# Kernel tuning notes

Hardware: AMD Instinct MI355X
Metric: run time of the kernel (lower is better)

Reference implementation:

```python
import jax, jax.numpy as jnp
import numpy as np

B, DIN, HID, DOUT, E, TOPK = 8192, 1024, 2048, 1024, 8, 2
GHID = HID // 2  # gating hidden


def setup_inputs() -> dict:
    key = jax.random.key(0)
    ks = jax.random.split(key, 16)
    s = lambda fan_in: 1.0 / np.sqrt(fan_in)
    return {
        "x": jax.random.normal(ks[0], (B, DIN), dtype=jnp.float32),
        # stacked expert params, leading axis = expert
        "w1": jax.random.uniform(ks[1], (E, DIN, HID), jnp.float32, -s(DIN), s(DIN)),
        "b1": jax.random.uniform(ks[2], (E, HID), jnp.float32, -s(DIN), s(DIN)),
        "w2": jax.random.uniform(ks[3], (E, HID, HID), jnp.float32, -s(HID), s(HID)),
        "b2": jax.random.uniform(ks[4], (E, HID), jnp.float32, -s(HID), s(HID)),
        "w3": jax.random.uniform(ks[5], (E, HID, DOUT), jnp.float32, -s(HID), s(HID)),
        "b3": jax.random.uniform(ks[6], (E, DOUT), jnp.float32, -s(HID), s(HID)),
        "wp": jax.random.uniform(ks[7], (E, DIN, HID), jnp.float32, -s(DIN), s(DIN)),
        "bp": jax.random.uniform(ks[8], (E, HID), jnp.float32, -s(DIN), s(DIN)),
        # gating network: Linear(DIN, GHID) -> ReLU -> Linear(GHID, E)
        "gw1": jax.random.uniform(ks[9], (DIN, GHID), jnp.float32, -s(DIN), s(DIN)),
        "gb1": jax.random.uniform(ks[10], (GHID,), jnp.float32, -s(DIN), s(DIN)),
        "gw2": jax.random.uniform(ks[11], (GHID, E), jnp.float32, -s(GHID), s(GHID)),
        "gb2": jax.random.uniform(ks[12], (E,), jnp.float32, -s(GHID), s(GHID)),
    }


def reference(x, w1, b1, w2, b2, w3, b3, wp, bp, gw1, gb1, gw2, gb2):
    # gating: [B, E]
    gate_logits = jnp.maximum(x @ gw1 + gb1, 0.0) @ gw2 + gb2
    topk_w, topk_i = jax.lax.top_k(gate_logits, TOPK)  # [B, K]
    topk_w = jax.nn.softmax(topk_w, axis=1)
    # dense per-expert residual MLP (dropout is identity in eval mode)
    h = jnp.maximum(jnp.einsum('bi,eih->beh', x, w1) + b1, 0.0)  # [B,E,HID]
    out = jnp.einsum('beh,ehg->beg', h, w2) + b2                  # [B,E,HID]
    identity = jnp.einsum('bi,eih->beh', x, wp) + bp              # projection
    out = jnp.maximum(out + identity, 0.0)
    expert_out = jnp.einsum('beh,eho->beo', out, w3) + b3         # [B,E,DOUT]
    # scatter top-k weights into dense [B, E] gate
    gate = jnp.zeros_like(gate_logits).at[jnp.arange(x.shape[0])[:, None], topk_i].set(topk_w)
    return jnp.einsum('beo,be->bo', expert_out, gate)             # [B, DOUT]
```

## Files before the change

### kernel.cpp

```cpp
#include <hip/hip_runtime.h>
#include <hip/hip_bf16.h>
#include <cstdint>
#include <cstddef>

#define TOK  8192
#define DIN  1024
#define HID  2048
#define DOUTN 1024
#define NEXP 8
#define GHID 1024

typedef __attribute__((ext_vector_type(8))) short bf16x8;
typedef __attribute__((ext_vector_type(4))) float floatx4;

__device__ __forceinline__ unsigned short f2b(float f) {
  unsigned int u = __float_as_uint(f);
  u += 0x7fffu + ((u >> 16) & 1u);
  return (unsigned short)(u >> 16);
}

__device__ __forceinline__ void async_cp16(const unsigned short* g, char* lds) {
  __builtin_amdgcn_global_load_lds(
      (const __attribute__((address_space(1))) unsigned int*)g,
      (__attribute__((address_space(3))) unsigned int*)lds, 16, 0, 0);
}


__global__ void cvt_x_kernel(const float* __restrict__ src,
                             unsigned short* __restrict__ dst, int n4) {
  int i = blockIdx.x * blockDim.x + threadIdx.x;
  if (i >= n4) return;
  float4 v = ((const float4*)src)[i];
  ushort4 o;
  o.x = f2b(v.x); o.y = f2b(v.y); o.z = f2b(v.z); o.w = f2b(v.w);
  ((ushort4*)dst)[i] = o;
}

__global__ void cvt_transpose_kernel(const float* __restrict__ src,
                                     unsigned short* __restrict__ dst,
                                     int K, int N) {
  __shared__ float tile[32][33];
  long e = blockIdx.z;
  src += e * (long)K * N;
  dst += e * (long)K * N;
  int n0 = blockIdx.x * 32, k0 = blockIdx.y * 32;
  int x = threadIdx.x, y = threadIdx.y;
#pragma unroll
  for (int i = 0; i < 4; i++)
    tile[y + 8 * i][x] = src[(long)(k0 + y + 8 * i) * N + n0 + x];
  __syncthreads();
#pragma unroll
  for (int i = 0; i < 4; i++)
    dst[(long)(n0 + y + 8 * i) * K + k0 + x] = f2b(tile[x][y + 8 * i]);
}


__global__ __launch_bounds__(256) void gating_sgemm(
    const float* __restrict__ X, const float* __restrict__ W,
    const float* __restrict__ bias, float* __restrict__ H) {
  __shared__ float As[8][128];
  __shared__ float Bs[8][128];
  int tid = threadIdx.x;
  int bm = blockIdx.y, bn = blockIdx.x;
  int tx = tid & 15, ty = tid >> 4;

  float acc[8][8] = {};
  int arow = tid >> 1;
  int acol = (tid & 1) * 4;
  int brow = tid >> 5;
  int bcol = (tid & 31) * 4;
  const float* Xp = X + (size_t)(bm * 128 + arow) * DIN + acol;
  const float* Wp = W + (size_t)brow * GHID + bn * 128 + bcol;

  for (int k0 = 0; k0 < DIN; k0 += 8) {
    float4 av = *(const float4*)(Xp + k0);
    float4 bv = *(const float4*)(Wp + (size_t)k0 * GHID);
    __syncthreads();
    As[acol + 0][arow] = av.x;
    As[acol + 1][arow] = av.y;
    As[acol + 2][arow] = av.z;
    As[acol + 3][arow] = av.w;
    *(float4*)&Bs[brow][bcol] = bv;
    __syncthreads();
#pragma unroll
    for (int k = 0; k < 8; ++k) {
      float ar[8], br[8];
      *(float4*)&ar[0] = *(const float4*)&As[k][ty * 4];
      *(float4*)&ar[4] = *(const float4*)&As[k][64 + ty * 4];
      *(float4*)&br[0] = *(const float4*)&Bs[k][tx * 4];
      *(float4*)&br[4] = *(const float4*)&Bs[k][64 + tx * 4];
#pragma unroll
      for (int i = 0; i < 8; ++i)
#pragma unroll
        for (int j = 0; j < 8; ++j) acc[i][j] += ar[i] * br[j];
    }
  }

#pragma unroll
  for (int hn = 0; hn < 2; ++hn) {
    int c0 = bn * 128 + hn * 64 + tx * 4;
    float4 bb = *(const float4*)(bias + c0);
#pragma unroll
    for (int hm = 0; hm < 2; ++hm)
#pragma unroll
      for (int i = 0; i < 4; ++i) {
        int m = bm * 128 + hm * 64 + ty * 4 + i;
        float4 v;
        v.x = fmaxf(acc[hm * 4 + i][hn * 4 + 0] + bb.x, 0.f);
        v.y = fmaxf(acc[hm * 4 + i][hn * 4 + 1] + bb.y, 0.f);
        v.z = fmaxf(acc[hm * 4 + i][hn * 4 + 2] + bb.z, 0.f);
        v.w = fmaxf(acc[hm * 4 + i][hn * 4 + 3] + bb.w, 0.f);
        *(float4*)(H + (size_t)m * GHID + c0) = v;
      }
  }
}


__global__ void gating2_topk(const float* __restrict__ H,
                             const float* __restrict__ gw2,
                             const float* __restrict__ gb2,
                             int* __restrict__ gidx, float* __restrict__ gwt) {
  int wv = threadIdx.x >> 6, lane = threadIdx.x & 63;
  int t = blockIdx.x * 4 + wv;
  const float* hrow = H + (size_t)t * GHID;
  float acc[8] = {};
  for (int k = lane; k < GHID; k += 64) {
    float v = hrow[k];
    float4 g0 = *(const float4*)(gw2 + (size_t)k * 8);
    float4 g1 = *(const float4*)(gw2 + (size_t)k * 8 + 4);
    acc[0] += v * g0.x; acc[1] += v * g0.y; acc[2] += v * g0.z; acc[3] += v * g0.w;
    acc[4] += v * g1.x; acc[5] += v * g1.y; acc[6] += v * g1.z; acc[7] += v * g1.w;
  }
#pragma unroll
  for (int off = 32; off > 0; off >>= 1)
#pragma unroll
    for (int e = 0; e < 8; e++) acc[e] += __shfl_xor(acc[e], off);

  if (lane == 0) {
    float l[8];
#pragma unroll
    for (int e = 0; e < 8; e++) l[e] = acc[e] + gb2[e];
    int b0 = 0; float v0 = l[0];
#pragma unroll
    for (int e = 1; e < 8; e++) if (l[e] > v0) { v0 = l[e]; b0 = e; }
    int b1 = -1; float v1 = -3.4e38f;
#pragma unroll
    for (int e = 0; e < 8; e++)
      if (e != b0 && l[e] > v1) { v1 = l[e]; b1 = e; }
    float ex = expf(v1 - v0);
    float inv = 1.f / (1.f + ex);
    gidx[2 * t] = b0; gidx[2 * t + 1] = b1;
    gwt[2 * t] = inv; gwt[2 * t + 1] = ex * inv;
  }
}


__global__ void route_count(const int* __restrict__ gidx, int* cnt) {
  int t = blockIdx.x * blockDim.x + threadIdx.x;
  int lane = threadIdx.x & 63;
  int e0 = gidx[2 * t], e1 = gidx[2 * t + 1];
#pragma unroll 1
  for (int e = 0; e < NEXP; e++) {
    unsigned long long m0 = __ballot(e0 == e);
    if (m0 && lane == __ffsll(m0) - 1) atomicAdd(&cnt[e], (int)__popcll(m0));
    unsigned long long m1 = __ballot(e1 == e);
    if (m1 && lane == __ffsll(m1) - 1) atomicAdd(&cnt[e], (int)__popcll(m1));
  }
}

__global__ void route_scan(const int* __restrict__ cnt, int* base_, int* cur) {
  if (threadIdx.x == 0) {
    int s = 0;
    for (int e = 0; e < NEXP; e++) { base_[e] = s; cur[e] = s; s += cnt[e]; }
  }
}

__global__ void route_scatter(const int* __restrict__ gidx,
                              const float* __restrict__ gwt, int* cur,
                              int* __restrict__ rt, float* __restrict__ rw) {
  int t = blockIdx.x * blockDim.x + threadIdx.x;
  int lane = threadIdx.x & 63;
  int e0 = gidx[2 * t], e1 = gidx[2 * t + 1];
  float w0 = gwt[2 * t], w1 = gwt[2 * t + 1];
#pragma unroll 1
  for (int e = 0; e < NEXP; e++) {
#pragma unroll 1
    for (int s = 0; s < 2; s++) {
      int mye = s ? e1 : e0;
      unsigned long long m = __ballot(mye == e);
      if (m) {
        int leader = __ffsll(m) - 1;
        int bb = 0;
        if (lane == leader) bb = atomicAdd(&cur[e], (int)__popcll(m));
        bb = __shfl(bb, leader);
        if (mye == e) {
          int pos = bb + (int)__popcll(m & ((1ull << lane) - 1ull));
          rt[pos] = t;
          rw[pos] = s ? w1 : w0;
        }
      }
    }
  }
}


template <int MODE>
__global__ __launch_bounds__(256, 2) void moe_gemm(
    const unsigned short* __restrict__ xb, const unsigned short* __restrict__ hbuf,
    const unsigned short* __restrict__ obuf, const unsigned short* __restrict__ w1t,
    const unsigned short* __restrict__ wpt, const unsigned short* __restrict__ w2t,
    const unsigned short* __restrict__ w3t, const float* __restrict__ b1,
    const float* __restrict__ b2, const float* __restrict__ bp,
    const float* __restrict__ b3, const int* __restrict__ rt,
    const float* __restrict__ rw, const int* __restrict__ cnt,
    const int* __restrict__ base, unsigned short* __restrict__ hout,
    unsigned short* __restrict__ oout, float* __restrict__ dout) {
  __shared__ __align__(16) unsigned short As[128 * 32];
  __shared__ __align__(16) unsigned short Bs[128 * 32];
  int tid = threadIdx.x;

  int lt = blockIdx.y;
  int e = 0, cn = 0, ok = 0;
  for (e = 0; e < NEXP; ++e) {
    int c = cnt[e];
    int nt = (c + 127) >> 7;
    if (lt < nt) { cn = c; ok = 1; break; }
    lt -= nt;
  }
  if (!ok) return;
  int be = base[e];
  int row0 = lt << 7;
  int tn = blockIdx.x << 7;

  int sr = tid >> 2;
  int lchunk = (tid & 3) ^ ((sr >> 1) & 3);
  int koffA = lchunk * 8;
  int rl0 = row0 + sr, rl1 = row0 + 64 + sr;
  int cl0 = min(rl0, cn - 1), cl1 = min(rl1, cn - 1);

  const unsigned short *a0p, *a1p, *a0q = nullptr, *a1q = nullptr;
  const unsigned short *bw0, *bw1, *bw0q = nullptr, *bw1q = nullptr;
  int KT;
  if (MODE == 1) {
    a0p = xb + (size_t)rt[be + cl0] * DIN + koffA;
    a1p = xb + (size_t)rt[be + cl1] * DIN + koffA;
    bw0 = w1t + ((size_t)e * HID + tn + sr) * DIN + koffA;
    bw1 = w1t + ((size_t)e * HID + tn + 64 + sr) * DIN + koffA;
    KT = DIN / 32;
  } else if (MODE == 2) {
    a0p = hbuf + (size_t)(be + cl0) * HID + koffA;
    a1p = hbuf + (size_t)(be + cl1) * HID + koffA;
    a0q = xb + (size_t)rt[be + cl0] * DIN + koffA;
    a1q = xb + (size_t)rt[be + cl1] * DIN + koffA;
    bw0 = w2t + (size_t)e * HID * HID + (size_t)(tn + sr) * HID + koffA;
    bw1 = w2t + (size_t)e * HID * HID + (size_t)(tn + 64 + sr) * HID + koffA;
    bw0q = wpt + (size_t)e * HID * DIN + (size_t)(tn + sr) * DIN + koffA;
    bw1q = wpt + (size_t)e * HID * DIN + (size_t)(tn + 64 + sr) * DIN + koffA;
    KT = (HID + DIN) / 32;
  } else {
    a0p = obuf + (size_t)(be + cl0) * HID + koffA;
    a1p = obuf + (size_t)(be + cl1) * HID + koffA;
    bw0 = w3t + (size_t)e * DOUTN * HID + (size_t)(tn + sr) * HID + koffA;
    bw1 = w3t + (size_t)e * DOUTN * HID + (size_t)(tn + 64 + sr) * HID + koffA;
    KT = HID / 32;
  }

  char* ldsA0 = (char*)As + (tid & 192) * 16;
  char* ldsB0 = (char*)Bs + (tid & 192) * 16;

  int lane = tid & 63, wv = tid >> 6;
  int wm = (wv >> 1) << 6, wn = (wv & 1) << 6;
  int q = lane >> 4, l15 = lane & 15;
  int abase = l15 * 64 + ((q ^ ((l15 >> 1) & 3)) << 4);
  const char* AsB = (const char*)As + wm * 64 + abase;
  const char* BsB = (const char*)Bs + wn * 64 + abase;

  floatx4 acc[4][4] = {};

  for (int kt = 0; kt < KT; ++kt) {
    int k0 = kt * 32;
    const unsigned short *pa0, *pa1, *pb0, *pb1;
    if (MODE == 2 && k0 >= HID) {
      int kk = k0 - HID;
      pa0 = a0q + kk; pa1 = a1q + kk; pb0 = bw0q + kk; pb1 = bw1q + kk;
    } else {
      pa0 = a0p + k0; pa1 = a1p + k0; pb0 = bw0 + k0; pb1 = bw1 + k0;
    }
    __syncthreads();
    async_cp16(pa0, ldsA0);
    async_cp16(pa1, ldsA0 + 4096);
    async_cp16(pb0, ldsB0);
    async_cp16(pb1, ldsB0 + 4096);
    __syncthreads();
    bf16x8 af[4], bfr[4];
#pragma unroll
    for (int i = 0; i < 4; i++) {
      af[i] = *(const bf16x8*)(AsB + i * 1024);
      bfr[i] = *(const bf16x8*)(BsB + i * 1024);
    }
#pragma unroll
    for (int mi = 0; mi < 4; mi++)
#pragma unroll
      for (int ni = 0; ni < 4; ni++)
        acc[mi][ni] = __builtin_amdgcn_mfma_f32_16x16x32_bf16(
            af[mi], bfr[ni], acc[mi][ni], 0, 0, 0);
  }

  int crow = row0 + wm + q * 4;
  int ccol0 = tn + wn + l15;
  if (MODE == 1) {
    const float* bb = b1 + (size_t)e * HID;
#pragma unroll
    for (int ni = 0; ni < 4; ++ni) {
      int col = ccol0 + ni * 16;
      float bias = bb[col];
#pragma unroll
      for (int mi = 0; mi < 4; ++mi)
#pragma unroll
        for (int rg = 0; rg < 4; ++rg) {
          int rr = crow + mi * 16 + rg;
          if (rr < cn) {
            float v = fmaxf(acc[mi][ni][rg] + bias, 0.f);
            hout[(size_t)(be + rr) * HID + col] = f2b(v);
          }
        }
    }
  } else if (MODE == 2) {
    const float* bb = b2 + (size_t)e * HID;
    const float* bq = bp + (size_t)e * HID;
#pragma unroll
    for (int ni = 0; ni < 4; ++ni) {
      int col = ccol0 + ni * 16;
      float bias = bb[col] + bq[col];
#pragma unroll
      for (int mi = 0; mi < 4; ++mi)
#pragma unroll
        for (int rg = 0; rg < 4; ++rg) {
          int rr = crow + mi * 16 + rg;
          if (rr < cn) {
            float v = fmaxf(acc[mi][ni][rg] + bias, 0.f);
            oout[(size_t)(be + rr) * HID + col] = f2b(v);
          }
        }
    }
  } else {
    const float* bb = b3 + (size_t)e * DOUTN;
    float biasv[4];
#pragma unroll
    for (int ni = 0; ni < 4; ++ni) biasv[ni] = bb[ccol0 + ni * 16];
#pragma unroll
    for (int mi = 0; mi < 4; ++mi)
#pragma unroll
      for (int rg = 0; rg < 4; ++rg) {
        int rr = crow + mi * 16 + rg;
        if (rr < cn) {
          int tk = rt[be + rr];
          float wgt = rw[be + rr];
#pragma unroll
          for (int ni = 0; ni < 4; ++ni) {
            int col = ccol0 + ni * 16;
            atomicAdd(dout + (size_t)tk * DOUTN + col,
                      (acc[mi][ni][rg] + biasv[ni]) * wgt);
          }
        }
      }
  }
}


extern "C" void kernel_launch(void* const* d_in, const int* in_sizes, int n_in,
                              void* d_out, int out_size, void* d_ws,
                              size_t ws_size, hipStream_t stream) {
  const float* x = (const float*)d_in[0];
  const float* w1 = (const float*)d_in[1];
  const float* b1 = (const float*)d_in[2];
  const float* w2 = (const float*)d_in[3];
  const float* b2 = (const float*)d_in[4];
  const float* w3 = (const float*)d_in[5];
  const float* b3 = (const float*)d_in[6];
  const float* wp = (const float*)d_in[7];
  const float* bp = (const float*)d_in[8];
  const float* gw1 = (const float*)d_in[9];
  const float* gb1 = (const float*)d_in[10];
  const float* gw2 = (const float*)d_in[11];
  const float* gb2 = (const float*)d_in[12];
  float* outp = (float*)d_out;
  char* ws = (char*)d_ws;

  const size_t o_w1t = 0;
  const size_t o_wpt = o_w1t + (size_t)NEXP * HID * DIN * 2;
  const size_t o_w2t = o_wpt + (size_t)NEXP * HID * DIN * 2;
  const size_t o_w3t = o_w2t + (size_t)NEXP * HID * HID * 2;
  const size_t o_xb  = o_w3t + (size_t)NEXP * DOUTN * HID * 2;
  const size_t o_hg  = o_xb + (size_t)TOK * DIN * 2;
  const size_t o_h   = o_hg + (size_t)TOK * GHID * 4;
  const size_t o_ob  = o_h + (size_t)2 * TOK * HID * 2;
  const size_t o_gidx = o_ob + (size_t)2 * TOK * HID * 2;
  const size_t o_gw  = o_gidx + (size_t)2 * TOK * 4;
  const size_t o_cnt = o_gw + (size_t)2 * TOK * 4;
  const size_t o_base = o_cnt + 128;
  const size_t o_cur = o_base + 128;
  const size_t o_rt  = o_cur + 128;
  const size_t o_rw  = o_rt + (size_t)2 * TOK * 4;

  unsigned short* w1t = (unsigned short*)(ws + o_w1t);
  unsigned short* wpt = (unsigned short*)(ws + o_wpt);
  unsigned short* w2t = (unsigned short*)(ws + o_w2t);
  unsigned short* w3t = (unsigned short*)(ws + o_w3t);
  unsigned short* xb = (unsigned short*)(ws + o_xb);
  float* hg = (float*)(ws + o_hg);
  unsigned short* hbuf = (unsigned short*)(ws + o_h);
  unsigned short* obuf = (unsigned short*)(ws + o_ob);
  int* gidx = (int*)(ws + o_gidx);
  float* gwt = (float*)(ws + o_gw);
  int* cnt = (int*)(ws + o_cnt);
  int* basep = (int*)(ws + o_base);
  int* cur = (int*)(ws + o_cur);
  int* rtl = (int*)(ws + o_rt);
  float* rwl = (float*)(ws + o_rw);

  hipMemsetAsync(d_out, 0, (size_t)out_size * 4, stream);
  hipMemsetAsync(ws + o_cnt, 0, 32, stream);

  cvt_x_kernel<<<dim3(TOK * DIN / 4 / 256), 256, 0, stream>>>(x, xb, TOK * DIN / 4);
  cvt_transpose_kernel<<<dim3(HID / 32, DIN / 32, NEXP), dim3(32, 8), 0, stream>>>(w1, w1t, DIN, HID);
  cvt_transpose_kernel<<<dim3(HID / 32, DIN / 32, NEXP), dim3(32, 8), 0, stream>>>(wp, wpt, DIN, HID);
  cvt_transpose_kernel<<<dim3(HID / 32, HID / 32, NEXP), dim3(32, 8), 0, stream>>>(w2, w2t, HID, HID);
  cvt_transpose_kernel<<<dim3(DOUTN / 32, HID / 32, NEXP), dim3(32, 8), 0, stream>>>(w3, w3t, HID, DOUTN);

  gating_sgemm<<<dim3(GHID / 128, TOK / 128), 256, 0, stream>>>(x, gw1, gb1, hg);
  gating2_topk<<<dim3(TOK / 4), 256, 0, stream>>>(hg, gw2, gb2, gidx, gwt);
  route_count<<<dim3(TOK / 256), 256, 0, stream>>>(gidx, cnt);
  route_scan<<<1, 64, 0, stream>>>(cnt, basep, cur);
  route_scatter<<<dim3(TOK / 256), 256, 0, stream>>>(gidx, gwt, cur, rtl, rwl);

  moe_gemm<1><<<dim3(HID / 128, 135), 256, 0, stream>>>(
      xb, hbuf, obuf, w1t, wpt, w2t, w3t, b1, b2, bp, b3, rtl, rwl, cnt, basep,
      hbuf, obuf, outp);
  moe_gemm<2><<<dim3(HID / 128, 135), 256, 0, stream>>>(
      xb, hbuf, obuf, w1t, wpt, w2t, w3t, b1, b2, bp, b3, rtl, rwl, cnt, basep,
      hbuf, obuf, outp);
  moe_gemm<3><<<dim3(DOUTN / 128, 135), 256, 0, stream>>>(
      xb, hbuf, obuf, w1t, wpt, w2t, w3t, b1, b2, bp, b3, rtl, rwl, cnt, basep,
      hbuf, obuf, outp);
}
```

Before: 1.230 ms.

## Run gating GEMM on MFMA using split-bf16 three-term emulation of fp32

Replaces the fp32 SIMT gating GEMM with an MFMA bf16 GEMM. x and gw1 are each split into hi and lo bf16 parts and concatenated along K as [hi,hi,lo] against [hi,lo,hi], so the three products approximate the fp32 result while keeping top-k routing stable. The main expert GEMM loop is also refactored into a shared macro, and MODE 2 becomes two separate loops instead of a per-iteration branch. This adds conversion kernels, a K three times as long, and workspace aliasing over the hbuf/obuf buffers.

```diff
diff --git a/kernel.cpp b/kernel.cpp
--- a/kernel.cpp
+++ b/kernel.cpp
@@ -19,6 +19,10 @@
   return (unsigned short)(u >> 16);
 }
 
+__device__ __forceinline__ float b2f(unsigned short b) {
+  return __uint_as_float(((unsigned int)b) << 16);
+}
+
 __device__ __forceinline__ void async_cp16(const unsigned short* g, char* lds) {
   __builtin_amdgcn_global_load_lds(
       (const __attribute__((address_space(1))) unsigned int*)g,
@@ -27,13 +31,23 @@
 
 
 __global__ void cvt_x_kernel(const float* __restrict__ src,
-                             unsigned short* __restrict__ dst, int n4) {
+                             unsigned short* __restrict__ xb,
+                             unsigned short* __restrict__ xcat, int n4) {
   int i = blockIdx.x * blockDim.x + threadIdx.x;
   if (i >= n4) return;
   float4 v = ((const float4*)src)[i];
-  ushort4 o;
-  o.x = f2b(v.x); o.y = f2b(v.y); o.z = f2b(v.z); o.w = f2b(v.w);
-  ((ushort4*)dst)[i] = o;
+  ushort4 hi, lo;
+  hi.x = f2b(v.x); lo.x = f2b(v.x - b2f(hi.x));
+  hi.y = f2b(v.y); lo.y = f2b(v.y - b2f(hi.y));
+  hi.z = f2b(v.z); lo.z = f2b(v.z - b2f(hi.z));
+  hi.w = f2b(v.w); lo.w = f2b(v.w - b2f(hi.w));
+  ((ushort4*)xb)[i] = hi;
+  int t = i >> 8;
+  int kk = i & 255;
+  ushort4* rowc = (ushort4*)(xcat + (size_t)t * 3072);
+  rowc[kk] = hi;
+  rowc[256 + kk] = hi;
+  rowc[512 + kk] = lo;
 }
 
 __global__ void cvt_transpose_kernel(const float* __restrict__ src,
@@ -54,63 +68,91 @@
     dst[(long)(n0 + y + 8 * i) * K + k0 + x] = f2b(tile[x][y + 8 * i]);
 }
 
-
-__global__ __launch_bounds__(256) void gating_sgemm(
-    const float* __restrict__ X, const float* __restrict__ W,
-    const float* __restrict__ bias, float* __restrict__ H) {
-  __shared__ float As[8][128];
-  __shared__ float Bs[8][128];
-  int tid = threadIdx.x;
-  int bm = blockIdx.y, bn = blockIdx.x;
-  int tx = tid & 15, ty = tid >> 4;
-
-  float acc[8][8] = {};
-  int arow = tid >> 1;
-  int acol = (tid & 1) * 4;
-  int brow = tid >> 5;
-  int bcol = (tid & 31) * 4;
-  const float* Xp = X + (size_t)(bm * 128 + arow) * DIN + acol;
-  const float* Wp = W + (size_t)brow * GHID + bn * 128 + bcol;
-
-  for (int k0 = 0; k0 < DIN; k0 += 8) {
-    float4 av = *(const float4*)(Xp + k0);
-    float4 bv = *(const float4*)(Wp + (size_t)k0 * GHID);
-    __syncthreads();
-    As[acol + 0][arow] = av.x;
-    As[acol + 1][arow] = av.y;
-    As[acol + 2][arow] = av.z;
-    As[acol + 3][arow] = av.w;
-    *(float4*)&Bs[brow][bcol] = bv;
-    __syncthreads();
-#pragma unroll
-    for (int k = 0; k < 8; ++k) {
-      float ar[8], br[8];
-      *(float4*)&ar[0] = *(const float4*)&As[k][ty * 4];
-      *(float4*)&ar[4] = *(const float4*)&As[k][64 + ty * 4];
-      *(float4*)&br[0] = *(const float4*)&Bs[k][tx * 4];
-      *(float4*)&br[4] = *(const float4*)&Bs[k][64 + tx * 4];
-#pragma unroll
-      for (int i = 0; i < 8; ++i)
-#pragma unroll
-        for (int j = 0; j < 8; ++j) acc[i][j] += ar[i] * br[j];
-    }
-  }
-
-#pragma unroll
-  for (int hn = 0; hn < 2; ++hn) {
-    int c0 = bn * 128 + hn * 64 + tx * 4;
-    float4 bb = *(const float4*)(bias + c0);
-#pragma unroll
-    for (int hm = 0; hm < 2; ++hm)
-#pragma unroll
-      for (int i = 0; i < 4; ++i) {
-        int m = bm * 128 + hm * 64 + ty * 4 + i;
-        float4 v;
-        v.x = fmaxf(acc[hm * 4 + i][hn * 4 + 0] + bb.x, 0.f);
-        v.y = fmaxf(acc[hm * 4 + i][hn * 4 + 1] + bb.y, 0.f);
-        v.z = fmaxf(acc[hm * 4 + i][hn * 4 + 2] + bb.z, 0.f);
-        v.w = fmaxf(acc[hm * 4 + i][hn * 4 + 3] + bb.w, 0.f);
-        *(float4*)(H + (size_t)m * GHID + c0) = v;
+__global__ void cvt_gw1_kernel(const float* __restrict__ src,
+                               unsigned short* __restrict__ dst) {
+  __shared__ float tile[32][33];
+  int n0 = blockIdx.x * 32, k0 = blockIdx.y * 32;
+  int x = threadIdx.x, y = threadIdx.y;
+#pragma unroll
+  for (int i = 0; i < 4; i++)
+    tile[y + 8 * i][x] = src[(long)(k0 + y + 8 * i) * GHID + n0 + x];
+  __syncthreads();
+#pragma unroll
+  for (int i = 0; i < 4; i++) {
+    float v = tile[x][y + 8 * i];
+    unsigned short hi = f2b(v);
+    unsigned short lo = f2b(v - b2f(hi));
+    size_t r = (size_t)(n0 + y + 8 * i) * 3072 + k0 + x;
+    dst[r] = hi;
+    dst[r + 1024] = lo;
+    dst[r + 2048] = hi;
+  }
+}
+
+
+#define KLOOP(pa0, pa1, pb0, pb1, NKT)                                        \
+  for (int kt = 0; kt < (NKT); ++kt) {                                        \
+    __syncthreads();                                                          \
+    async_cp16((pa0) + kt * 32, ldsA0);                                       \
+    async_cp16((pa1) + kt * 32, ldsA0 + 4096);                                \
+    async_cp16((pb0) + kt * 32, ldsB0);                                       \
+    async_cp16((pb1) + kt * 32, ldsB0 + 4096);                                \
+    __syncthreads();                                                          \
+    bf16x8 af[4], bfr[4];                                                     \
+    _Pragma("unroll") for (int i = 0; i < 4; i++) {                           \
+      af[i] = *(const bf16x8*)(AsB + i * 1024);                               \
+      bfr[i] = *(const bf16x8*)(BsB + i * 1024);                              \
+    }                                                                         \
+    _Pragma("unroll") for (int mi = 0; mi < 4; mi++)                          \
+      _Pragma("unroll") for (int ni = 0; ni < 4; ni++)                        \
+        acc[mi][ni] = __builtin_amdgcn_mfma_f32_16x16x32_bf16(                \
+            af[mi], bfr[ni], acc[mi][ni], 0, 0, 0);                           \
+  }
+
+#define TILE_SETUP()                                                          \
+  int tid = threadIdx.x;                                                      \
+  int sr = tid >> 2;                                                          \
+  int lchunk = (tid & 3) ^ ((sr >> 1) & 3);                                   \
+  int koffA = lchunk * 8;                                                     \
+  char* ldsA0 = (char*)As + (tid & 192) * 16;                                 \
+  char* ldsB0 = (char*)Bs + (tid & 192) * 16;                                 \
+  int lane = tid & 63, wv = tid >> 6;                                         \
+  int wm = (wv >> 1) << 6, wn = (wv & 1) << 6;                                \
+  int q = lane >> 4, l15 = lane & 15;                                         \
+  int abase = l15 * 64 + ((q ^ ((l15 >> 1) & 3)) << 4);                       \
+  const char* AsB = (const char*)As + wm * 64 + abase;                        \
+  const char* BsB = (const char*)Bs + wn * 64 + abase;                        \
+  floatx4 acc[4][4] = {};
+
+
+__global__ __launch_bounds__(256, 2) void gating_mfma(
+    const unsigned short* __restrict__ xcat,
+    const unsigned short* __restrict__ gw1t3,
+    const float* __restrict__ gb1, float* __restrict__ H) {
+  __shared__ __align__(16) unsigned short As[128 * 32];
+  __shared__ __align__(16) unsigned short Bs[128 * 32];
+  TILE_SETUP();
+  int row0 = blockIdx.y << 7, tn = blockIdx.x << 7;
+
+  const unsigned short* a0p = xcat + (size_t)(row0 + sr) * 3072 + koffA;
+  const unsigned short* a1p = xcat + (size_t)(row0 + 64 + sr) * 3072 + koffA;
+  const unsigned short* b0p = gw1t3 + (size_t)(tn + sr) * 3072 + koffA;
+  const unsigned short* b1p = gw1t3 + (size_t)(tn + 64 + sr) * 3072 + koffA;
+
+  KLOOP(a0p, a1p, b0p, b1p, 3072 / 32);
+
+  int crow = row0 + wm + q * 4;
+  int ccol0 = tn + wn + l15;
+#pragma unroll
+  for (int ni = 0; ni < 4; ++ni) {
+    int col = ccol0 + ni * 16;
+    float bias = gb1[col];
+#pragma unroll
+    for (int mi = 0; mi < 4; ++mi)
+#pragma unroll
+      for (int rg = 0; rg < 4; ++rg) {
+        int rr = crow + mi * 16 + rg;
+        H[(size_t)rr * GHID + col] = fmaxf(acc[mi][ni][rg] + bias, 0.f);
       }
   }
 }
@@ -217,7 +259,6 @@
     unsigned short* __restrict__ oout, float* __restrict__ dout) {
   __shared__ __align__(16) unsigned short As[128 * 32];
   __shared__ __align__(16) unsigned short Bs[128 * 32];
-  int tid = threadIdx.x;
 
   int lt = blockIdx.y;
   int e = 0, cn = 0, ok = 0;
@@ -232,78 +273,34 @@
   int row0 = lt << 7;
   int tn = blockIdx.x << 7;
 
-  int sr = tid >> 2;
-  int lchunk = (tid & 3) ^ ((sr >> 1) & 3);
-  int koffA = lchunk * 8;
+  TILE_SETUP();
+
   int rl0 = row0 + sr, rl1 = row0 + 64 + sr;
   int cl0 = min(rl0, cn - 1), cl1 = min(rl1, cn - 1);
 
-  const unsigned short *a0p, *a1p, *a0q = nullptr, *a1q = nullptr;
-  const unsigned short *bw0, *bw1, *bw0q = nullptr, *bw1q = nullptr;
-  int KT;
   if (MODE == 1) {
-    a0p = xb + (size_t)rt[be + cl0] * DIN + koffA;
-    a1p = xb + (size_t)rt[be + cl1] * DIN + koffA;
-    bw0 = w1t + ((size_t)e * HID + tn + sr) * DIN + koffA;
-    bw1 = w1t + ((size_t)e * HID + tn + 64 + sr) * DIN + koffA;
-    KT = DIN / 32;
+    const unsigned short* a0p = xb + (size_t)rt[be + cl0] * DIN + koffA;
+    const unsigned short* a1p = xb + (size_t)rt[be + cl1] * DIN + koffA;
+    const unsigned short* bw0 = w1t + ((size_t)e * HID + tn + sr) * DIN + koffA;
+    const unsigned short* bw1 = w1t + ((size_t)e * HID + tn + 64 + sr) * DIN + koffA;
+    KLOOP(a0p, a1p, bw0, bw1, DIN / 32);
   } else if (MODE == 2) {
-    a0p = hbuf + (size_t)(be + cl0) * HID + koffA;
-    a1p = hbuf + (size_t)(be + cl1) * HID + koffA;
-    a0q = xb + (size_t)rt[be + cl0] * DIN + koffA;
-    a1q = xb + (size_t)rt[be + cl1] * DIN + koffA;
-    bw0 = w2t + (size_t)e * HID * HID + (size_t)(tn + sr) * HID + koffA;
-    bw1 = w2t + (size_t)e * HID * HID + (size_t)(tn + 64 + sr) * HID + koffA;
-    bw0q = wpt + (size_t)e * HID * DIN + (size_t)(tn + sr) * DIN + koffA;
-    bw1q = wpt + (size_t)e * HID * DIN + (size_t)(tn + 64 + sr) * DIN + koffA;
-    KT = (HID + DIN) / 32;
+    const unsigned short* a0p = hbuf + (size_t)(be + cl0) * HID + koffA;
+    const unsigned short* a1p = hbuf + (size_t)(be + cl1) * HID + koffA;
+    const unsigned short* bw0 = w2t + (size_t)e * HID * HID + (size_t)(tn + sr) * HID + koffA;
+    const unsigned short* bw1 = w2t + (size_t)e * HID * HID + (size_t)(tn + 64 + sr) * HID + koffA;
+    KLOOP(a0p, a1p, bw0, bw1, HID / 32);
+    const unsigned short* a0q = xb + (size_t)rt[be + cl0] * DIN + koffA;
+    const unsigned short* a1q = xb + (size_t)rt[be + cl1] * DIN + koffA;
+    const unsigned short* bq0 = wpt + (size_t)e * HID * DIN + (size_t)(tn + sr) * DIN + koffA;
+    const unsigned short* bq1 = wpt + (size_t)e * HID * DIN + (size_t)(tn + 64 + sr) * DIN + koffA;
+    KLOOP(a0q, a1q, bq0, bq1, DIN / 32);
   } else {
-    a0p = obuf + (size_t)(be + cl0) * HID + koffA;
-    a1p = obuf + (size_t)(be + cl1) * HID + koffA;
-    bw0 = w3t + (size_t)e * DOUTN * HID + (size_t)(tn + sr) * HID + koffA;
-    bw1 = w3t + (size_t)e * DOUTN * HID + (size_t)(tn + 64 + sr) * HID + koffA;
-    KT = HID / 32;
-  }
-
-  char* ldsA0 = (char*)As + (tid & 192) * 16;
-  char* ldsB0 = (char*)Bs + (tid & 192) * 16;
-
-  int lane = tid & 63, wv = tid >> 6;
-  int wm = (wv >> 1) << 6, wn = (wv & 1) << 6;
-  int q = lane >> 4, l15 = lane & 15;
-  int abase = l15 * 64 + ((q ^ ((l15 >> 1) & 3)) << 4);
-  const char* AsB = (const char*)As + wm * 64 + abase;
-  const char* BsB = (const char*)Bs + wn * 64 + abase;
-
-  floatx4 acc[4][4] = {};
-
-  for (int kt = 0; kt < KT; ++kt) {
-    int k0 = kt * 32;
-    const unsigned short *pa0, *pa1, *pb0, *pb1;
-    if (MODE == 2 && k0 >= HID) {
-      int kk = k0 - HID;
-      pa0 = a0q + kk; pa1 = a1q + kk; pb0 = bw0q + kk; pb1 = bw1q + kk;
-    } else {
-      pa0 = a0p + k0; pa1 = a1p + k0; pb0 = bw0 + k0; pb1 = bw1 + k0;
-    }
-    __syncthreads();
-    async_cp16(pa0, ldsA0);
-    async_cp16(pa1, ldsA0 + 4096);
-    async_cp16(pb0, ldsB0);
-    async_cp16(pb1, ldsB0 + 4096);
-    __syncthreads();
-    bf16x8 af[4], bfr[4];
-#pragma unroll
-    for (int i = 0; i < 4; i++) {
-      af[i] = *(const bf16x8*)(AsB + i * 1024);
-      bfr[i] = *(const bf16x8*)(BsB + i * 1024);
-    }
-#pragma unroll
-    for (int mi = 0; mi < 4; mi++)
-#pragma unroll
-      for (int ni = 0; ni < 4; ni++)
-        acc[mi][ni] = __builtin_amdgcn_mfma_f32_16x16x32_bf16(
-            af[mi], bfr[ni], acc[mi][ni], 0, 0, 0);
+    const unsigned short* a0p = obuf + (size_t)(be + cl0) * HID + koffA;
+    const unsigned short* a1p = obuf + (size_t)(be + cl1) * HID + koffA;
+    const unsigned short* bw0 = w3t + (size_t)e * DOUTN * HID + (size_t)(tn + sr) * HID + koffA;
+    const unsigned short* bw1 = w3t + (size_t)e * DOUTN * HID + (size_t)(tn + 64 + sr) * HID + koffA;
+    KLOOP(a0p, a1p, bw0, bw1, HID / 32);
   }
 
   int crow = row0 + wm + q * 4;
@@ -402,6 +399,8 @@
   const size_t o_cur = o_base + 128;
   const size_t o_rt  = o_cur + 128;
   const size_t o_rw  = o_rt + (size_t)2 * TOK * 4;
+  const size_t o_xcat = o_ob;
+  const size_t o_gw1t3 = o_h;
 
   unsigned short* w1t = (unsigned short*)(ws + o_w1t);
   unsigned short* wpt = (unsigned short*)(ws + o_wpt);
@@ -411,6 +410,8 @@
   float* hg = (float*)(ws + o_hg);
   unsigned short* hbuf = (unsigned short*)(ws + o_h);
   unsigned short* obuf = (unsigned short*)(ws + o_ob);
+  unsigned short* xcat = (unsigned short*)(ws + o_xcat);
+  unsigned short* gw1t3 = (unsigned short*)(ws + o_gw1t3);
   int* gidx = (int*)(ws + o_gidx);
   float* gwt = (float*)(ws + o_gw);
   int* cnt = (int*)(ws + o_cnt);
@@ -422,13 +423,14 @@
   hipMemsetAsync(d_out, 0, (size_t)out_size * 4, stream);
   hipMemsetAsync(ws + o_cnt, 0, 32, stream);
 
-  cvt_x_kernel<<<dim3(TOK * DIN / 4 / 256), 256, 0, stream>>>(x, xb, TOK * DIN / 4);
+  cvt_x_kernel<<<dim3(TOK * DIN / 4 / 256), 256, 0, stream>>>(x, xb, xcat, TOK * DIN / 4);
+  cvt_gw1_kernel<<<dim3(GHID / 32, DIN / 32), dim3(32, 8), 0, stream>>>(gw1, gw1t3);
   cvt_transpose_kernel<<<dim3(HID / 32, DIN / 32, NEXP), dim3(32, 8), 0, stream>>>(w1, w1t, DIN, HID);
   cvt_transpose_kernel<<<dim3(HID / 32, DIN / 32, NEXP), dim3(32, 8), 0, stream>>>(wp, wpt, DIN, HID);
   cvt_transpose_kernel<<<dim3(HID / 32, HID / 32, NEXP), dim3(32, 8), 0, stream>>>(w2, w2t, HID, HID);
   cvt_transpose_kernel<<<dim3(DOUTN / 32, HID / 32, NEXP), dim3(32, 8), 0, stream>>>(w3, w3t, HID, DOUTN);
 
-  gating_sgemm<<<dim3(GHID / 128, TOK / 128), 256, 0, stream>>>(x, gw1, gb1, hg);
+  gating_mfma<<<dim3(GHID / 128, TOK / 128), 256, 0, stream>>>(xcat, gw1t3, gb1, hg);
   gating2_topk<<<dim3(TOK / 4), 256, 0, stream>>>(hg, gw2, gb2, gidx, gwt);
   route_count<<<dim3(TOK / 256), 256, 0, stream>>>(gidx, cnt);
   route_scan<<<1, 64, 0, stream>>>(cnt, basep, cur);
```

New measurement: 1.123 ms. 1.09x faster.
